# Kernel tuning notes

Hardware: AMD Instinct MI355X
Metric: run time of the kernel (lower is better)

The kernel has to match this reference:

```python
import jax, jax.numpy as jnp
import numpy as np

def setup_inputs() -> dict:
    key = jax.random.key(0)
    k1, k2 = jax.random.split(key)
    user_embeddings = jax.random.normal(k1, (1024, 64), dtype=jnp.float32)
    movie_embeddings = jax.random.normal(k2, (50000, 64), dtype=jnp.float32)
    return {"user_embeddings": user_embeddings, "movie_embeddings": movie_embeddings}

def reference(user_embeddings, movie_embeddings):
    # square_of_sum[b,m] = (sum_k u[b,k] m[m,k])^2
    square_of_sum = jnp.matmul(user_embeddings, movie_embeddings.T) ** 2
    # sum_of_square[b,m] = sum_k (u[b,k] m[m,k])^2 = (u^2) @ (m^2)^T
    # Algebraically identical to the original's broadcast (B, M, D) intermediate,
    # but computed as a second GEMM on squared embeddings.
    sum_of_square = jnp.matmul(user_embeddings ** 2, (movie_embeddings ** 2).T)
    interaction = 0.5 * (square_of_sum - sum_of_square)
    return interaction
```

## Files before the change

kernel.cpp:

```cpp
#include <hip/hip_runtime.h>

typedef short short8 __attribute__((ext_vector_type(8)));
typedef float f32x4 __attribute__((ext_vector_type(4)));

#define DK 64
#define BM 64
#define BN 128

__device__ __forceinline__ short f2bf(float x) {
    unsigned u = __builtin_bit_cast(unsigned, x);
    unsigned r = (u + 0x7fffu + ((u >> 16) & 1u)) >> 16;
    return (short)r;
}

__device__ __forceinline__ void gl_lds16(const void* g, void* l) {
    __builtin_amdgcn_global_load_lds(
        (const __attribute__((address_space(1))) unsigned int*)g,
        (__attribute__((address_space(3))) unsigned int*)l, 16, 0, 0);
}

__global__ __launch_bounds__(256)
void fm_convert(const float* __restrict__ U, const float* __restrict__ M,
                short* __restrict__ ws, int NU, int NM, int NUP, int NMP) {
    int id = blockIdx.x * blockDim.x + threadIdx.x;
    int total = (NUP + NMP) * 8;
    if (id >= total) return;
    int rowg = id >> 3;
    int p = id & 7;
    const float* src; short *dv, *dq; int row, nvalid;
    if (rowg < NUP) {
        row = rowg; src = U; dv = ws; dq = ws + (size_t)NUP * DK; nvalid = NU;
    } else {
        row = rowg - NUP; src = M;
        dv = ws + (size_t)2 * NUP * DK; dq = dv + (size_t)NMP * DK; nvalid = NM;
    }
    short8 v8 = {0,0,0,0,0,0,0,0}, q8 = {0,0,0,0,0,0,0,0};
    if (row < nvalid) {
        const int cp = p ^ (row & 7);
        const float* s = src + (size_t)row * DK + cp * 8;
        float4 a = *(const float4*)(s);
        float4 b = *(const float4*)(s + 4);
        v8 = (short8){ f2bf(a.x), f2bf(a.y), f2bf(a.z), f2bf(a.w),
                       f2bf(b.x), f2bf(b.y), f2bf(b.z), f2bf(b.w) };
        q8 = (short8){ f2bf(a.x*a.x), f2bf(a.y*a.y), f2bf(a.z*a.z), f2bf(a.w*a.w),
                       f2bf(b.x*b.x), f2bf(b.y*b.y), f2bf(b.z*b.z), f2bf(b.w*b.w) };
    }
    *(short8*)(dv + (size_t)row * DK + p * 8) = v8;
    *(short8*)(dq + (size_t)row * DK + p * 8) = q8;
}

__global__ __launch_bounds__(256, 3)
void fm_gemm(const short* __restrict__ ws, float* __restrict__ out,
             int NM, int NMP, int NUP) {
    __shared__ short sA [BM * DK];
    __shared__ short sA2[BM * DK];
    __shared__ short sB [BN * DK];
    __shared__ short sB2[BN * DK];

    const int t = threadIdx.x;
    const int lane = t & 63;
    const int w = t >> 6;
    const int lr = lane & 15;
    const int lk = lane >> 4;

    const int ub  = blockIdx.x * BM;
    const int nb0 = blockIdx.y * BN;

    const short* gU  = ws;
    const short* gU2 = ws + (size_t)NUP * DK;
    const short* gM  = ws + (size_t)2 * NUP * DK;
    const short* gM2 = gM + (size_t)NMP * DK;

    {
        const short* srcA  = gU  + (size_t)ub * DK;
        const short* srcA2 = gU2 + (size_t)ub * DK;
        const short* srcB  = gM  + (size_t)nb0 * DK;
        const short* srcB2 = gM2 + (size_t)nb0 * DK;
        const int lo = lane * 8;
#pragma unroll
        for (int j = 0; j < 2; ++j) {
            const int ch = w * 2 + j;
            gl_lds16(srcA  + ch * 512 + lo, &sA [ch * 512]);
            gl_lds16(srcA2 + ch * 512 + lo, &sA2[ch * 512]);
        }
#pragma unroll
        for (int j = 0; j < 4; ++j) {
            const int ch = w * 4 + j;
            gl_lds16(srcB  + ch * 512 + lo, &sB [ch * 512]);
            gl_lds16(srcB2 + ch * 512 + lo, &sB2[ch * 512]);
        }
    }
    __syncthreads();

    short8 av[4][2], aq[4][2];
#pragma unroll
    for (int m = 0; m < 4; ++m)
#pragma unroll
        for (int ks = 0; ks < 2; ++ks) {
            const int row = m * 16 + lr;
            const int c = ks * 4 + lk;
            const int idx = row * DK + ((c ^ (row & 7)) << 3);
            av[m][ks] = *(const short8*)&sA [idx];
            aq[m][ks] = *(const short8*)&sA2[idx];
        }
    short8 bv[2][2], bq[2][2];
#pragma unroll
    for (int n = 0; n < 2; ++n)
#pragma unroll
        for (int ks = 0; ks < 2; ++ks) {
            const int row = w * 32 + n * 16 + lr;
            const int c = ks * 4 + lk;
            const int idx = row * DK + ((c ^ (row & 7)) << 3);
            bv[n][ks] = *(const short8*)&sB [idx];
            bq[n][ks] = *(const short8*)&sB2[idx];
        }

    f32x4 s[4][2], qa[4][2];
#pragma unroll
    for (int m = 0; m < 4; ++m)
#pragma unroll
        for (int n = 0; n < 2; ++n) {
            s[m][n]  = (f32x4){0.f, 0.f, 0.f, 0.f};
            qa[m][n] = (f32x4){0.f, 0.f, 0.f, 0.f};
        }

#pragma unroll
    for (int m = 0; m < 4; ++m)
#pragma unroll
        for (int n = 0; n < 2; ++n)
#pragma unroll
            for (int ks = 0; ks < 2; ++ks) {
                s[m][n]  = __builtin_amdgcn_mfma_f32_16x16x32_bf16(bv[n][ks], av[m][ks], s[m][n],  0, 0, 0);
                qa[m][n] = __builtin_amdgcn_mfma_f32_16x16x32_bf16(bq[n][ks], aq[m][ks], qa[m][n], 0, 0, 0);
            }

    const int nbW = nb0 + w * 32;
#pragma unroll
    for (int m = 0; m < 4; ++m) {
        float* rowp = out + (size_t)(ub + m * 16 + lr) * NM;
#pragma unroll
        for (int n = 0; n < 2; ++n) {
            const int col = nbW + n * 16 + lk * 4;
            if (col < NM) {
                f32x4 sv = s[m][n], qv = qa[m][n];
                f32x4 rr;
#pragma unroll
                for (int j = 0; j < 4; ++j)
                    rr[j] = 0.5f * (sv[j] * sv[j] - qv[j]);
                *(f32x4*)(rowp + col) = rr;
            }
        }
    }
}

__global__ __launch_bounds__(256, 2)
void fm_fallback(const float* __restrict__ U, const float* __restrict__ M,
                 float* __restrict__ out, int NU, int NM) {
    __shared__ short sA [128 * DK];
    __shared__ short sA2[128 * DK];
    __shared__ short sB [128 * DK];
    __shared__ short sB2[128 * DK];

    const int t = threadIdx.x;
    const int lane = t & 63;
    const int w = t >> 6;
    const int wr = w >> 1;
    const int wc = w & 1;
    const int lr = lane & 15;
    const int lk = lane >> 4;

    const int mbase = blockIdx.x * 128;
    const int nbase = blockIdx.y * 128;

    const int r0 = t >> 4;
    const int c4 = t & 15;
    const int chunk = c4 >> 1;
    const int sub = c4 & 1;

    typedef short short4v __attribute__((ext_vector_type(4)));
#pragma unroll
    for (int i = 0; i < 8; ++i) {
        const int r = r0 + i * 16;
        const int sidx = r * DK + ((chunk ^ (r & 7)) << 3) + (sub << 2);
        {
            float4 v = make_float4(0.f, 0.f, 0.f, 0.f);
            const int gr = mbase + r;
            if (gr < NU) v = *(const float4*)(U + (size_t)gr * DK + c4 * 4);
            short4v b  = { f2bf(v.x), f2bf(v.y), f2bf(v.z), f2bf(v.w) };
            short4v b2 = { f2bf(v.x*v.x), f2bf(v.y*v.y), f2bf(v.z*v.z), f2bf(v.w*v.w) };
            *(short4v*)&sA[sidx] = b; *(short4v*)&sA2[sidx] = b2;
        }
        {
            float4 v = make_float4(0.f, 0.f, 0.f, 0.f);
            const int gr = nbase + r;
            if (gr < NM) v = *(const float4*)(M + (size_t)gr * DK + c4 * 4);
            short4v b  = { f2bf(v.x), f2bf(v.y), f2bf(v.z), f2bf(v.w) };
            short4v b2 = { f2bf(v.x*v.x), f2bf(v.y*v.y), f2bf(v.z*v.z), f2bf(v.w*v.w) };
            *(short4v*)&sB[sidx] = b; *(short4v*)&sB2[sidx] = b2;
        }
    }
    __syncthreads();

    f32x4 accS[4][4], accQ[4][4];
#pragma unroll
    for (int m = 0; m < 4; ++m)
#pragma unroll
        for (int n = 0; n < 4; ++n) {
            accS[m][n] = (f32x4){0.f,0.f,0.f,0.f};
            accQ[m][n] = (f32x4){0.f,0.f,0.f,0.f};
        }
#pragma unroll
    for (int ks = 0; ks < 2; ++ks) {
        short8 af[4], a2f[4], bfr[4], b2f[4];
        const int c = ks * 4 + lk;
#pragma unroll
        for (int m = 0; m < 4; ++m) {
            const int row = wr * 64 + m * 16 + lr;
            const int idx = row * DK + ((c ^ (row & 7)) << 3);
            af[m] = *(const short8*)&sA[idx]; a2f[m] = *(const short8*)&sA2[idx];
        }
#pragma unroll
        for (int n = 0; n < 4; ++n) {
            const int row = wc * 64 + n * 16 + lr;
            const int idx = row * DK + ((c ^ (row & 7)) << 3);
            bfr[n] = *(const short8*)&sB[idx]; b2f[n] = *(const short8*)&sB2[idx];
        }
#pragma unroll
        for (int m = 0; m < 4; ++m)
#pragma unroll
            for (int n = 0; n < 4; ++n) {
                accS[m][n] = __builtin_amdgcn_mfma_f32_16x16x32_bf16(af[m],  bfr[n], accS[m][n], 0, 0, 0);
                accQ[m][n] = __builtin_amdgcn_mfma_f32_16x16x32_bf16(a2f[m], b2f[n], accQ[m][n], 0, 0, 0);
            }
    }
#pragma unroll
    for (int m = 0; m < 4; ++m) {
        const int grow0 = mbase + wr * 64 + m * 16 + lk * 4;
#pragma unroll
        for (int n = 0; n < 4; ++n) {
            const int gcol = nbase + wc * 64 + n * 16 + lr;
            if (gcol < NM) {
                f32x4 s = accS[m][n]; f32x4 q = accQ[m][n];
#pragma unroll
                for (int r = 0; r < 4; ++r) {
                    const int grow = grow0 + r;
                    if (grow < NU)
                        out[(size_t)grow * NM + gcol] = 0.5f * (s[r]*s[r] - q[r]);
                }
            }
        }
    }
}

extern "C" void kernel_launch(void* const* d_in, const int* in_sizes, int n_in,
                              void* d_out, int out_size, void* d_ws, size_t ws_size,
                              hipStream_t stream) {
    const float* U = (const float*)d_in[0];
    const float* M = (const float*)d_in[1];
    float* out = (float*)d_out;
    const int NU = in_sizes[0] / DK;
    const int NM = in_sizes[1] / DK;
    const int NUP = NU;
    const int NMP = ((NM + BN - 1) / BN) * BN;
    const size_t need = (size_t)(NUP + NMP) * DK * 2 * sizeof(short);

    if ((NU % BM == 0) && (NM % 4 == 0) && ws_size >= need) {
        short* ws = (short*)d_ws;
        const int tasks = (NUP + NMP) * 8;
        fm_convert<<<(tasks + 255) / 256, 256, 0, stream>>>(U, M, ws, NU, NM, NUP, NMP);
        dim3 grid(NU / BM, NMP / BN);
        fm_gemm<<<grid, dim3(256), 0, stream>>>(ws, out, NM, NMP, NUP);
    } else {
        dim3 grid((NU + 127) / 128, (NM + 127) / 128);
        fm_fallback<<<grid, dim3(256), 0, stream>>>(U, M, out, NU, NM);
    }
}
```

Measured before the change: 60.75 us.

## Square bf16 embeddings in-register instead of storing squared copies

The convert kernel now writes only the bf16 embeddings, and the GEMM computes the squared operands from the loaded bf16 values, rounding back to bf16. This halves workspace writes and reads plus LDS usage, which allows a higher occupancy hint (5 blocks). The output stage is restructured per m-row to shrink accumulator register use. The squared values now come from bf16-rounded inputs rather than the original fp32, which slightly changes numerics.

```diff
diff --git a/kernel.cpp b/kernel.cpp
--- a/kernel.cpp
+++ b/kernel.cpp
@@ -11,6 +11,18 @@
     unsigned u = __builtin_bit_cast(unsigned, x);
     unsigned r = (u + 0x7fffu + ((u >> 16) & 1u)) >> 16;
     return (short)r;
+}
+
+__device__ __forceinline__ short8 sq8(short8 v) {
+    short8 r;
+#pragma unroll
+    for (int i = 0; i < 8; ++i) {
+        unsigned u = ((unsigned)(unsigned short)v[i]) << 16;
+        float f = __builtin_bit_cast(float, u);
+        unsigned p = __builtin_bit_cast(unsigned, f * f);
+        r[i] = (short)((p + 0x8000u) >> 16);
+    }
+    return r;
 }
 
 __device__ __forceinline__ void gl_lds16(const void* g, void* l) {
@@ -27,14 +39,14 @@
     if (id >= total) return;
     int rowg = id >> 3;
     int p = id & 7;
-    const float* src; short *dv, *dq; int row, nvalid;
+    const float* src; short* dv; int row, nvalid;
     if (rowg < NUP) {
-        row = rowg; src = U; dv = ws; dq = ws + (size_t)NUP * DK; nvalid = NU;
+        row = rowg; src = U; dv = ws; nvalid = NU;
     } else {
         row = rowg - NUP; src = M;
-        dv = ws + (size_t)2 * NUP * DK; dq = dv + (size_t)NMP * DK; nvalid = NM;
-    }
-    short8 v8 = {0,0,0,0,0,0,0,0}, q8 = {0,0,0,0,0,0,0,0};
+        dv = ws + (size_t)NUP * DK; nvalid = NM;
+    }
+    short8 v8 = {0,0,0,0,0,0,0,0};
     if (row < nvalid) {
         const int cp = p ^ (row & 7);
         const float* s = src + (size_t)row * DK + cp * 8;
@@ -42,20 +54,15 @@
         float4 b = *(const float4*)(s + 4);
         v8 = (short8){ f2bf(a.x), f2bf(a.y), f2bf(a.z), f2bf(a.w),
                        f2bf(b.x), f2bf(b.y), f2bf(b.z), f2bf(b.w) };
-        q8 = (short8){ f2bf(a.x*a.x), f2bf(a.y*a.y), f2bf(a.z*a.z), f2bf(a.w*a.w),
-                       f2bf(b.x*b.x), f2bf(b.y*b.y), f2bf(b.z*b.z), f2bf(b.w*b.w) };
     }
     *(short8*)(dv + (size_t)row * DK + p * 8) = v8;
-    *(short8*)(dq + (size_t)row * DK + p * 8) = q8;
-}
-
-__global__ __launch_bounds__(256, 3)
+}
+
+__global__ __launch_bounds__(256, 5)
 void fm_gemm(const short* __restrict__ ws, float* __restrict__ out,
              int NM, int NMP, int NUP) {
-    __shared__ short sA [BM * DK];
-    __shared__ short sA2[BM * DK];
-    __shared__ short sB [BN * DK];
-    __shared__ short sB2[BN * DK];
+    __shared__ short sA[BM * DK];
+    __shared__ short sB[BN * DK];
 
     const int t = threadIdx.x;
     const int lane = t & 63;
@@ -66,43 +73,26 @@
     const int ub  = blockIdx.x * BM;
     const int nb0 = blockIdx.y * BN;
 
-    const short* gU  = ws;
-    const short* gU2 = ws + (size_t)NUP * DK;
-    const short* gM  = ws + (size_t)2 * NUP * DK;
-    const short* gM2 = gM + (size_t)NMP * DK;
+    const short* gU = ws;
+    const short* gM = ws + (size_t)NUP * DK;
 
     {
-        const short* srcA  = gU  + (size_t)ub * DK;
-        const short* srcA2 = gU2 + (size_t)ub * DK;
-        const short* srcB  = gM  + (size_t)nb0 * DK;
-        const short* srcB2 = gM2 + (size_t)nb0 * DK;
+        const short* srcA = gU + (size_t)ub * DK;
+        const short* srcB = gM + (size_t)nb0 * DK;
         const int lo = lane * 8;
 #pragma unroll
         for (int j = 0; j < 2; ++j) {
             const int ch = w * 2 + j;
-            gl_lds16(srcA  + ch * 512 + lo, &sA [ch * 512]);
-            gl_lds16(srcA2 + ch * 512 + lo, &sA2[ch * 512]);
+            gl_lds16(srcA + ch * 512 + lo, &sA[ch * 512]);
         }
 #pragma unroll
         for (int j = 0; j < 4; ++j) {
             const int ch = w * 4 + j;
-            gl_lds16(srcB  + ch * 512 + lo, &sB [ch * 512]);
-            gl_lds16(srcB2 + ch * 512 + lo, &sB2[ch * 512]);
+            gl_lds16(srcB + ch * 512 + lo, &sB[ch * 512]);
         }
     }
     __syncthreads();
 
-    short8 av[4][2], aq[4][2];
-#pragma unroll
-    for (int m = 0; m < 4; ++m)
-#pragma unroll
-        for (int ks = 0; ks < 2; ++ks) {
-            const int row = m * 16 + lr;
-            const int c = ks * 4 + lk;
-            const int idx = row * DK + ((c ^ (row & 7)) << 3);
-            av[m][ks] = *(const short8*)&sA [idx];
-            aq[m][ks] = *(const short8*)&sA2[idx];
-        }
     short8 bv[2][2], bq[2][2];
 #pragma unroll
     for (int n = 0; n < 2; ++n)
@@ -111,38 +101,45 @@
             const int row = w * 32 + n * 16 + lr;
             const int c = ks * 4 + lk;
             const int idx = row * DK + ((c ^ (row & 7)) << 3);
-            bv[n][ks] = *(const short8*)&sB [idx];
-            bq[n][ks] = *(const short8*)&sB2[idx];
-        }
-
-    f32x4 s[4][2], qa[4][2];
-#pragma unroll
-    for (int m = 0; m < 4; ++m)
+            bv[n][ks] = *(const short8*)&sB[idx];
+            bq[n][ks] = sq8(bv[n][ks]);
+        }
+
+    const int nbW = nb0 + w * 32;
+
+#pragma unroll
+    for (int m = 0; m < 4; ++m) {
+        short8 av0, av1, aq0, aq1;
+        {
+            const int row = m * 16 + lr;
+            const int i0 = row * DK + (((0 * 4 + lk) ^ (row & 7)) << 3);
+            const int i1 = row * DK + (((1 * 4 + lk) ^ (row & 7)) << 3);
+            av0 = *(const short8*)&sA[i0];
+            av1 = *(const short8*)&sA[i1];
+            aq0 = sq8(av0);
+            aq1 = sq8(av1);
+        }
+
+        f32x4 s[2], q[2];
 #pragma unroll
         for (int n = 0; n < 2; ++n) {
-            s[m][n]  = (f32x4){0.f, 0.f, 0.f, 0.f};
-            qa[m][n] = (f32x4){0.f, 0.f, 0.f, 0.f};
-        }
-
-#pragma unroll
-    for (int m = 0; m < 4; ++m)
-#pragma unroll
-        for (int n = 0; n < 2; ++n)
-#pragma unroll
-            for (int ks = 0; ks < 2; ++ks) {
-                s[m][n]  = __builtin_amdgcn_mfma_f32_16x16x32_bf16(bv[n][ks], av[m][ks], s[m][n],  0, 0, 0);
-                qa[m][n] = __builtin_amdgcn_mfma_f32_16x16x32_bf16(bq[n][ks], aq[m][ks], qa[m][n], 0, 0, 0);
-            }
-
-    const int nbW = nb0 + w * 32;
-#pragma unroll
-    for (int m = 0; m < 4; ++m) {
+            s[n] = (f32x4){0.f, 0.f, 0.f, 0.f};
+            q[n] = (f32x4){0.f, 0.f, 0.f, 0.f};
+        }
+#pragma unroll
+        for (int n = 0; n < 2; ++n) {
+            s[n] = __builtin_amdgcn_mfma_f32_16x16x32_bf16(bv[n][0], av0, s[n], 0, 0, 0);
+            s[n] = __builtin_amdgcn_mfma_f32_16x16x32_bf16(bv[n][1], av1, s[n], 0, 0, 0);
+            q[n] = __builtin_amdgcn_mfma_f32_16x16x32_bf16(bq[n][0], aq0, q[n], 0, 0, 0);
+            q[n] = __builtin_amdgcn_mfma_f32_16x16x32_bf16(bq[n][1], aq1, q[n], 0, 0, 0);
+        }
+
         float* rowp = out + (size_t)(ub + m * 16 + lr) * NM;
 #pragma unroll
         for (int n = 0; n < 2; ++n) {
             const int col = nbW + n * 16 + lk * 4;
             if (col < NM) {
-                f32x4 sv = s[m][n], qv = qa[m][n];
+                f32x4 sv = s[n], qv = q[n];
                 f32x4 rr;
 #pragma unroll
                 for (int j = 0; j < 4; ++j)
@@ -262,7 +259,7 @@
     const int NM = in_sizes[1] / DK;
     const int NUP = NU;
     const int NMP = ((NM + BN - 1) / BN) * BN;
-    const size_t need = (size_t)(NUP + NMP) * DK * 2 * sizeof(short);
+    const size_t need = (size_t)(NUP + NMP) * DK * sizeof(short);
 
     if ((NU % BM == 0) && (NM % 4 == 0) && ws_size >= need) {
         short* ws = (short*)d_ws;
```

Measured after the change: 50.97 us. 1.19x faster.
